# Kernel optimization log

Hardware: AMD Instinct MI355X
Metric: run time of the kernel (lower is better)

Reference implementation:

```python
import jax, jax.numpy as jnp
import numpy as np

N, D, K = 65536, 512, 4096


def setup_inputs() -> dict:
    key = jax.random.key(0)
    kx, kc = jax.random.split(key)
    x = jax.random.normal(kx, (N, D), dtype=jnp.float32)
    center = jax.random.normal(kc, (K, D), dtype=jnp.float32)
    return {"x": x, "center": center}


def squared_euclidean(x, center):
    x_sq = jnp.sum(x * x, axis=1, keepdims=True)        # [N,1]
    c_sq = jnp.sum(center * center, axis=1)             # [K]
    cross = x @ center.T                                # [N,K] GEMM
    return x_sq - 2.0 * cross + c_sq[None, :]


def reference(x, center):
    # KMeans.forward: dis_func(input, center).argmin(1)
    dist = squared_euclidean(x, center)                 # [N,K]
    return jnp.argmin(dist, axis=1)                     # [N] int32
```

## Files before the change

### kernel.cpp

```cpp
#include <hip/hip_runtime.h>

#define N_ROWS 65536
#define DIM    512
#define K_CENT 4096
#define TILE_M 256
#define TILE_N 64
#define NCT    (K_CENT / TILE_N)
#define KSTEPS 8
#define THREADS 256
#define WCAP   1024
#define WTRIG  512
#define MARGIN 22.0f
#define SCALE1 0x7F7F7F7F

typedef float  floatx4  __attribute__((ext_vector_type(4)));
typedef float  floatx16 __attribute__((ext_vector_type(16)));
typedef int    intx4    __attribute__((ext_vector_type(4)));
typedef int    intx8    __attribute__((ext_vector_type(8)));

__device__ __forceinline__ unsigned mapF(float f) {
  unsigned u = __float_as_uint(f);
  return (u & 0x80000000u) ? ~u : (u | 0x80000000u);
}
__device__ __forceinline__ float unmapF(unsigned m) {
  unsigned u = (m & 0x80000000u) ? (m ^ 0x80000000u) : ~m;
  return __uint_as_float(u);
}

__device__ __forceinline__ void gload_lds16(const void* g, void* l) {
  __builtin_amdgcn_global_load_lds(
      (const __attribute__((address_space(1))) void*)g,
      (__attribute__((address_space(3))) void*)l, 16, 0, 0);
}

__device__ __forceinline__ int pk4(float a, float b, float c, float d) {
  int r = __builtin_amdgcn_cvt_pk_fp8_f32(a, b, 0, false);
  r = __builtin_amdgcn_cvt_pk_fp8_f32(c, d, r, true);
  return r;
}

#define WAVE_LDS_FENCE() do { asm volatile("s_waitcnt lgkmcnt(0)" ::: "memory"); \
                              __builtin_amdgcn_sched_barrier(0); } while (0)

__global__ void prep_convert(const float* __restrict__ c,
                             unsigned char* __restrict__ cq, float* __restrict__ csqg) {
  size_t i = ((size_t)blockIdx.x * blockDim.x + threadIdx.x) * 16;
  if (i >= (size_t)K_CENT * DIM) return;
  floatx4 a0 = *(const floatx4*)(c + i);
  floatx4 a1 = *(const floatx4*)(c + i + 4);
  floatx4 a2 = *(const floatx4*)(c + i + 8);
  floatx4 a3 = *(const floatx4*)(c + i + 12);
  intx4 q = { pk4(a0[0],a0[1],a0[2],a0[3]), pk4(a1[0],a1[1],a1[2],a1[3]),
              pk4(a2[0],a2[1],a2[2],a2[3]), pk4(a3[0],a3[1],a3[2],a3[3]) };
  *(intx4*)(cq + i) = q;
  float s = 0.f;
#pragma unroll
  for (int e = 0; e < 4; ++e)
    s += a0[e]*a0[e] + a1[e]*a1[e] + a2[e]*a2[e] + a3[e]*a3[e];
#pragma unroll
  for (int o = 1; o < 32; o <<= 1) s += __shfl_xor(s, o, 64);
  if ((threadIdx.x & 31) == 0) csqg[i >> 9] = s;
}

__global__ __launch_bounds__(THREADS, 1)
void kmeans_argmin_pipe(const float* __restrict__ x, const float* __restrict__ cent,
                        const unsigned char* __restrict__ cq,
                        const float* __restrict__ csqg, int* __restrict__ out) {
  __shared__ __align__(16) unsigned char ringLds[4][16384];
  __shared__ __align__(16) float csqL[K_CENT];
  __shared__ unsigned sminU[TILE_M];
  __shared__ unsigned long long best[TILE_M];
  __shared__ unsigned poolK[4][WCAP];
  __shared__ float    poolS[4][WCAP];
  __shared__ int candCnt[4];

  const int t = threadIdx.x;
  const int lane = t & 63;
  const int wave = t >> 6;
  const int l31 = lane & 31;
  const int half = lane >> 5;
  const int rowBlock = blockIdx.x * TILE_M;

  sminU[t] = 0xFFFFFFFFu;
  best[t] = ~0ull;
  if (t < 4) candCnt[t] = 0;
#pragma unroll
  for (int i = 0; i < K_CENT / THREADS; ++i) csqL[t + i * THREADS] = csqg[t + i * THREADS];

  int offI0, offI1, offI2, offI3;
#pragma unroll
  for (int i = 0; i < 4; ++i) {
    int s = i * 64 + lane;
    int rS = (s >> 2) & 31;
    int row = (s >> 7) * 32 + rS;
    int cp = (s & 3) ^ ((rS >> 1) & 3);
    int v = row * DIM + cp * 16;
    if (i == 0) offI0 = v; else if (i == 1) offI1 = v;
    else if (i == 2) offI2 = v; else offI3 = v;
  }

  const int qk = half * 2;
  const int slotLo = 4 * l31 + (qk ^ ((l31 >> 1) & 3));
  const int loB = slotLo * 16;
  const int hiB = (slotLo ^ 1) * 16;
  unsigned char* ringW = ringLds[wave];

  intx8 xfA[KSTEPS], xfB[KSTEPS];
  {
    const float* xr = x + (size_t)(rowBlock + wave * 64 + l31) * DIM + half * 32;
#pragma unroll
    for (int ks = 0; ks < KSTEPS; ++ks) {
      int q[8];
#pragma unroll
      for (int j = 0; j < 8; ++j) {
        floatx4 f = *(const floatx4*)(xr + ks * 64 + j * 4);
        q[j] = pk4(f[0], f[1], f[2], f[3]);
      }
      xfA[ks] = (intx8){q[0], q[1], q[2], q[3], q[4], q[5], q[6], q[7]};
    }
    xr += (size_t)32 * DIM;
#pragma unroll
    for (int ks = 0; ks < KSTEPS; ++ks) {
      int q[8];
#pragma unroll
      for (int j = 0; j < 8; ++j) {
        floatx4 f = *(const floatx4*)(xr + ks * 64 + j * 4);
        q[j] = pk4(f[0], f[1], f[2], f[3]);
      }
      xfB[ks] = (intx8){q[0], q[1], q[2], q[3], q[4], q[5], q[6], q[7]};
    }
  }

  __syncthreads();

#pragma unroll
  for (int s = 0; s < 3; ++s) {
    unsigned char* wb = ringW + (s << 12);
    gload_lds16(cq + s * 64 + offI0, wb);
    gload_lds16(cq + s * 64 + offI1, wb + 1024);
    gload_lds16(cq + s * 64 + offI2, wb + 2048);
    gload_lds16(cq + s * 64 + offI3, wb + 3072);
  }
  unsigned sOff = 3 * 64;

  for (int ct = 0; ct < NCT; ++ct) {
    floatx16 acc00, acc01, acc10, acc11;
#pragma unroll
    for (int e = 0; e < 16; ++e) { acc00[e] = 0.f; acc01[e] = 0.f; acc10[e] = 0.f; acc11[e] = 0.f; }

#pragma unroll
    for (int p = 0; p < KSTEPS; ++p) {
      {
        unsigned char* wb = ringW + (((p + 3) & 3) << 12);
        gload_lds16(cq + sOff + offI0, wb);
        gload_lds16(cq + sOff + offI1, wb + 1024);
        gload_lds16(cq + sOff + offI2, wb + 2048);
        gload_lds16(cq + sOff + offI3, wb + 3072);
      }
      sOff += (p == 4) ? 32320u : 64u;
      asm volatile("s_waitcnt vmcnt(12)" ::: "memory");
      __builtin_amdgcn_sched_barrier(0);

      const unsigned char* rb = ringW + ((p & 3) << 12);
      intx4 lo0 = *(const intx4*)(rb + loB);
      intx4 hi0 = *(const intx4*)(rb + hiB);
      intx4 lo1 = *(const intx4*)(rb + 2048 + loB);
      intx4 hi1 = *(const intx4*)(rb + 2048 + hiB);
      asm volatile("s_waitcnt lgkmcnt(0)" ::: "memory");
      __builtin_amdgcn_sched_barrier(0);
      intx8 b0 = (intx8){lo0[0],lo0[1],lo0[2],lo0[3], hi0[0],hi0[1],hi0[2],hi0[3]};
      intx8 b1 = (intx8){lo1[0],lo1[1],lo1[2],lo1[3], hi1[0],hi1[1],hi1[2],hi1[3]};
      acc00 = __builtin_amdgcn_mfma_scale_f32_32x32x64_f8f6f4(
          b0, xfA[p], acc00, 0, 0, 0, SCALE1, 0, SCALE1);
      acc01 = __builtin_amdgcn_mfma_scale_f32_32x32x64_f8f6f4(
          b1, xfA[p], acc01, 0, 0, 0, SCALE1, 0, SCALE1);
      acc10 = __builtin_amdgcn_mfma_scale_f32_32x32x64_f8f6f4(
          b0, xfB[p], acc10, 0, 0, 0, SCALE1, 0, SCALE1);
      acc11 = __builtin_amdgcn_mfma_scale_f32_32x32x64_f8f6f4(
          b1, xfB[p], acc11, 0, 0, 0, SCALE1, 0, SCALE1);
    }

    const int ctB = ct << 6;
#pragma unroll
    for (int h = 0; h < 2; ++h) {
      const floatx16& a0 = h ? acc10 : acc00;
      const floatx16& a1 = h ? acc11 : acc01;
      const int srow = wave * 64 + h * 32 + l31;
      float mn = 3.4e38f;
#pragma unroll
      for (int gg = 0; gg < 4; ++gg) {
        floatx4 c0 = *(const floatx4*)&csqL[ctB + 8 * gg + 4 * half];
        floatx4 c1 = *(const floatx4*)&csqL[ctB + 32 + 8 * gg + 4 * half];
#pragma unroll
        for (int e = 0; e < 4; ++e) {
          mn = fminf(mn, c0[e] - 2.f * a0[4 * gg + e]);
          mn = fminf(mn, c1[e] - 2.f * a1[4 * gg + e]);
        }
      }
      mn = fminf(mn, __shfl_xor(mn, 32, 64));
      if (half == 0) atomicMin(&sminU[srow], mapF(mn));
      WAVE_LDS_FENCE();

      const float thr = unmapF(sminU[srow]) + MARGIN;
#pragma unroll
      for (int gg = 0; gg < 4; ++gg) {
        floatx4 c0 = *(const floatx4*)&csqL[ctB + 8 * gg + 4 * half];
        floatx4 c1 = *(const floatx4*)&csqL[ctB + 32 + 8 * gg + 4 * half];
#pragma unroll
        for (int e = 0; e < 4; ++e) {
          float s0 = c0[e] - 2.f * a0[4 * gg + e];
          if (s0 <= thr) {
            int k = ctB + 8 * gg + 4 * half + e;
            int idx = atomicAdd(&candCnt[wave], 1);
            if (idx < WCAP) { poolK[wave][idx] = ((unsigned)k << 8) | (unsigned)srow; poolS[wave][idx] = s0; }
          }
          float s1 = c1[e] - 2.f * a1[4 * gg + e];
          if (s1 <= thr) {
            int k = ctB + 32 + 8 * gg + 4 * half + e;
            int idx = atomicAdd(&candCnt[wave], 1);
            if (idx < WCAP) { poolK[wave][idx] = ((unsigned)k << 8) | (unsigned)srow; poolS[wave][idx] = s1; }
          }
        }
      }
    }
    WAVE_LDS_FENCE();

    if (candCnt[wave] > WTRIG) {
      int cc = candCnt[wave]; if (cc > WCAP) cc = WCAP;
      unsigned myK[16]; float myS[16]; int myN = 0;
      for (int i = lane; i < cc; i += 64) {
        int rl = poolK[wave][i] & 255;
        if (poolS[wave][i] <= unmapF(sminU[rl]) + MARGIN) {
          myK[myN] = poolK[wave][i]; myS[myN] = poolS[wave][i]; ++myN;
        }
      }
      WAVE_LDS_FENCE();
      if (lane == 0) candCnt[wave] = 0;
      WAVE_LDS_FENCE();
      int base = atomicAdd(&candCnt[wave], myN);
      for (int j = 0; j < myN; ++j) { poolK[wave][base + j] = myK[j]; poolS[wave][base + j] = myS[j]; }
      WAVE_LDS_FENCE();
    }
  }

  __syncthreads();

  const int grp = t >> 4;
  const int sl = t & 15;
  for (int w = 0; w < 4; ++w) {
    int cw = candCnt[w]; if (cw > WCAP) cw = WCAP;
    for (int ci = grp; ci < cw; ci += 16) {
      unsigned cd = poolK[w][ci];
      int rl = cd & 255;
      if (poolS[w][ci] > unmapF(sminU[rl]) + MARGIN) continue;
      int k = cd >> 8;
      const float* xr = x + (size_t)(rowBlock + rl) * DIM;
      const float* cr = cent + (size_t)k * DIM;
      double d = 0.0;
#pragma unroll
      for (int jj = 0; jj < DIM / 64; ++jj) {
        floatx4 xv = *(const floatx4*)(xr + jj * 64 + sl * 4);
        floatx4 cv = *(const floatx4*)(cr + jj * 64 + sl * 4);
#pragma unroll
        for (int e = 0; e < 4; ++e) {
          double df = (double)xv[e] - (double)cv[e];
          d += df * df;
        }
      }
#pragma unroll
      for (int off = 1; off < 16; off <<= 1) d += __shfl_xor(d, off, 64);
      if (sl == 0) {
        unsigned long long key =
            ((unsigned long long)__double_as_longlong(d) & ~0xFFFull) | (unsigned long long)k;
        atomicMin(&best[rl], key);
      }
    }
  }
  __syncthreads();
  out[rowBlock + t] = (int)(best[t] & 0xFFFull);
}

#define FB_TILE_M 128
#define FB_NKT    32
#define FB_CAP    1536
#define FB_TRIG   1024
__global__ __launch_bounds__(512, 4)
void kmeans_argmin_fb(const float* __restrict__ x, const float* __restrict__ cent,
                      int* __restrict__ out) {
  __shared__ unsigned char ldsA[FB_TILE_M * 64];
  __shared__ unsigned char ldsB[128 * 64];
  __shared__ float csq4[128][4];
  __shared__ unsigned sminU[FB_TILE_M];
  __shared__ unsigned long long best[FB_TILE_M];
  __shared__ unsigned candKey[FB_CAP];
  __shared__ float candS[FB_CAP];
  __shared__ int candCount;

  const int t = threadIdx.x;
  const int lane = t & 63;
  const int wave = t >> 6;
  const int wm = wave >> 1;
  const int wn = wave & 1;
  const int l31 = lane & 31;
  const int half = lane >> 5;
  const int rowBlock = blockIdx.x * FB_TILE_M;

  if (t < FB_TILE_M) { sminU[t] = 0xFFFFFFFFu; best[t] = ~0ull; }
  if (t == 0) candCount = 0;

  const int rS = (t >> 2) & 31;
  const int rowS = (t >> 7) * 32 + rS;
  const int offS = (((t & 3) ^ ((rS >> 1) & 3)) << 4);
  const int qk = half * 2;
  const int fragSlotBase = 4 * l31 + (qk ^ ((l31 >> 1) & 3));

  for (int kt = 0; kt < FB_NKT; ++kt) {
    const int ktBase = kt * 128;
    ((float*)csq4)[t] = 0.f;
    floatx16 acc[2];
#pragma unroll
    for (int fn = 0; fn < 2; ++fn)
#pragma unroll
      for (int e = 0; e < 16; ++e) acc[fn][e] = 0.f;

    for (int ks = 0; ks < KSTEPS; ++ks) {
      const int kd = ks * 64;
      {
        const float* gA = x + (size_t)(rowBlock + rowS) * DIM + kd + offS;
        floatx4 f0 = *(const floatx4*)gA, f1 = *(const floatx4*)(gA + 4);
        floatx4 f2 = *(const floatx4*)(gA + 8), f3 = *(const floatx4*)(gA + 12);
        intx4 q = { pk4(f0[0],f0[1],f0[2],f0[3]), pk4(f1[0],f1[1],f1[2],f1[3]),
                    pk4(f2[0],f2[1],f2[2],f2[3]), pk4(f3[0],f3[1],f3[2],f3[3]) };
        *(intx4*)(ldsA + (size_t)t * 16) = q;
      }
      {
        const float* gB = cent + (size_t)(ktBase + rowS) * DIM + kd + offS;
        floatx4 f0 = *(const floatx4*)gB, f1 = *(const floatx4*)(gB + 4);
        floatx4 f2 = *(const floatx4*)(gB + 8), f3 = *(const floatx4*)(gB + 12);
        intx4 q = { pk4(f0[0],f0[1],f0[2],f0[3]), pk4(f1[0],f1[1],f1[2],f1[3]),
                    pk4(f2[0],f2[1],f2[2],f2[3]), pk4(f3[0],f3[1],f3[2],f3[3]) };
        *(intx4*)(ldsB + (size_t)t * 16) = q;
        float s = 0.f;
#pragma unroll
        for (int e = 0; e < 4; ++e)
          s += f0[e]*f0[e] + f1[e]*f1[e] + f2[e]*f2[e] + f3[e]*f3[e];
        csq4[rowS][t & 3] += s;
      }
      __syncthreads();

      intx8 aF, bF[2];
      {
        int s0 = wm * 128 + fragSlotBase;
        intx4 lo = *(const intx4*)(ldsA + s0 * 16);
        intx4 hi = *(const intx4*)(ldsA + (s0 ^ 1) * 16);
        aF = (intx8){lo[0], lo[1], lo[2], lo[3], hi[0], hi[1], hi[2], hi[3]};
      }
#pragma unroll
      for (int fn = 0; fn < 2; ++fn) {
        int s0 = (wn * 2 + fn) * 128 + fragSlotBase;
        intx4 lo = *(const intx4*)(ldsB + s0 * 16);
        intx4 hi = *(const intx4*)(ldsB + (s0 ^ 1) * 16);
        bF[fn] = (intx8){lo[0], lo[1], lo[2], lo[3], hi[0], hi[1], hi[2], hi[3]};
      }
#pragma unroll
      for (int fn = 0; fn < 2; ++fn)
        acc[fn] = __builtin_amdgcn_mfma_scale_f32_32x32x64_f8f6f4(
            aF, bF[fn], acc[fn], 0, 0, 0, SCALE1, 0, SCALE1);
      __syncthreads();
    }

    float cs[2];
#pragma unroll
    for (int fn = 0; fn < 2; ++fn) {
      int cl = wn * 64 + fn * 32 + l31;
      cs[fn] = csq4[cl][0] + csq4[cl][1] + csq4[cl][2] + csq4[cl][3];
    }

#pragma unroll
    for (int r = 0; r < 16; ++r) {
      float v = fminf(cs[0] - 2.f * acc[0][r], cs[1] - 2.f * acc[1][r]);
      v = fminf(v, __shfl_xor(v, 1, 64));
      v = fminf(v, __shfl_xor(v, 2, 64));
      v = fminf(v, __shfl_xor(v, 4, 64));
      v = fminf(v, __shfl_xor(v, 8, 64));
      v = fminf(v, __shfl_xor(v, 16, 64));
      if (l31 == 0) {
        int srow = wm * 32 + (r & 3) + 8 * (r >> 2) + 4 * half;
        atomicMin(&sminU[srow], mapF(v));
      }
    }
    __syncthreads();

#pragma unroll
    for (int r = 0; r < 16; ++r) {
      int srow = wm * 32 + (r & 3) + 8 * (r >> 2) + 4 * half;
      float thr = unmapF(sminU[srow]) + MARGIN;
#pragma unroll
      for (int fn = 0; fn < 2; ++fn) {
        float s = cs[fn] - 2.f * acc[fn][r];
        if (s <= thr) {
          int k = ktBase + wn * 64 + fn * 32 + l31;
          int idx = atomicAdd(&candCount, 1);
          if (idx < FB_CAP) {
            candKey[idx] = ((unsigned)k << 7) | (unsigned)srow;
            candS[idx] = s;
          }
        }
      }
    }
    __syncthreads();

    if (candCount > FB_TRIG) {
      int cc = candCount; if (cc > FB_CAP) cc = FB_CAP;
      unsigned myK[4]; float myS[4]; int myN = 0;
      for (int i = t; i < cc; i += 512) {
        int rl = candKey[i] & 127;
        if (candS[i] <= unmapF(sminU[rl]) + MARGIN && myN < 4) {
          myK[myN] = candKey[i]; myS[myN] = candS[i]; ++myN;
        }
      }
      __syncthreads();
      if (t == 0) candCount = 0;
      __syncthreads();
      int base = atomicAdd(&candCount, myN);
      for (int j = 0; j < myN; ++j) { candKey[base + j] = myK[j]; candS[base + j] = myS[j]; }
      __syncthreads();
    }
  }

  int cnt = candCount; if (cnt > FB_CAP) cnt = FB_CAP;
  const int g = t >> 4;
  const int sl = t & 15;
  for (int ci = g; ci < cnt; ci += 32) {
    unsigned cd = candKey[ci];
    int rl = cd & 127;
    if (candS[ci] > unmapF(sminU[rl]) + MARGIN) continue;
    int k = cd >> 7;
    const float* xr = x + (size_t)(rowBlock + rl) * DIM;
    const float* cr = cent + (size_t)k * DIM;
    double d = 0.0;
#pragma unroll
    for (int j = 0; j < DIM / 64; ++j) {
      floatx4 xv = *(const floatx4*)(xr + j * 64 + sl * 4);
      floatx4 cv = *(const floatx4*)(cr + j * 64 + sl * 4);
#pragma unroll
      for (int e = 0; e < 4; ++e) {
        double df = (double)xv[e] - (double)cv[e];
        d += df * df;
      }
    }
#pragma unroll
    for (int off = 1; off < 16; off <<= 1) d += __shfl_xor(d, off, 64);
    if (sl == 0) {
      unsigned long long key =
          ((unsigned long long)__double_as_longlong(d) & ~0xFFFull) | (unsigned long long)k;
      atomicMin(&best[rl], key);
    }
  }
  __syncthreads();
  if (t < FB_TILE_M) out[rowBlock + t] = (int)(best[t] & 0xFFFull);
}

extern "C" void kernel_launch(void* const* d_in, const int* in_sizes, int n_in,
                              void* d_out, int out_size, void* d_ws, size_t ws_size,
                              hipStream_t stream) {
  const float* x = (const float*)d_in[0];
  const float* cent = (const float*)d_in[1];
  int* out = (int*)d_out;
  const size_t nXq = (size_t)N_ROWS * DIM;
  const size_t nCq = (size_t)K_CENT * DIM;
  const size_t nCsq = (size_t)K_CENT * sizeof(float);

  if (ws_size >= nXq + nCq + nCsq) {
    unsigned char* cq = (unsigned char*)d_ws;
    float* csqg = (float*)(cq + nCq);
    const size_t total16 = nCq / 16;
    prep_convert<<<(unsigned)((total16 + 255) / 256), 256, 0, stream>>>(cent, cq, csqg);
    kmeans_argmin_pipe<<<N_ROWS / TILE_M, THREADS, 0, stream>>>(x, cent, cq, csqg, out);
  } else {
    kmeans_argmin_fb<<<N_ROWS / FB_TILE_M, 512, 0, stream>>>(x, cent, out);
  }
}
```

Baseline: 605.8 us.

## Load fp8 centroid fragments directly into registers and halve row tile

The per-wave LDS ring filled with global_load_lds is removed. Each lane now loads its centroid fp8 fragments straight from global memory into registers, double-buffered across k-steps. The row tile drops from 256 to 128 (32 rows per wave), and launch bounds allow two blocks per CU, which cuts register and LDS use to raise occupancy. The trade-off is that every wave re-reads the centroid tiles from global/L2 with no sharing, and each x row pair now gets half the reuse of each B fragment.

```diff
diff --git a/kernel.cpp b/kernel.cpp
--- a/kernel.cpp
+++ b/kernel.cpp
@@ -3,7 +3,7 @@
 #define N_ROWS 65536
 #define DIM    512
 #define K_CENT 4096
-#define TILE_M 256
+#define TILE_M 128
 #define TILE_N 64
 #define NCT    (K_CENT / TILE_N)
 #define KSTEPS 8
@@ -25,12 +25,6 @@
 __device__ __forceinline__ float unmapF(unsigned m) {
   unsigned u = (m & 0x80000000u) ? (m ^ 0x80000000u) : ~m;
   return __uint_as_float(u);
-}
-
-__device__ __forceinline__ void gload_lds16(const void* g, void* l) {
-  __builtin_amdgcn_global_load_lds(
-      (const __attribute__((address_space(1))) void*)g,
-      (__attribute__((address_space(3))) void*)l, 16, 0, 0);
 }
 
 __device__ __forceinline__ int pk4(float a, float b, float c, float d) {
@@ -62,11 +56,40 @@
   if ((threadIdx.x & 31) == 0) csqg[i >> 9] = s;
 }
 
-__global__ __launch_bounds__(THREADS, 1)
+#define LOADP(buf, p0, p1, kb) do {                                   \
+  buf[0] = *(const intx4*)((p0) + (kb) * 64);                         \
+  buf[1] = *(const intx4*)((p0) + (kb) * 64 + 16);                    \
+  buf[2] = *(const intx4*)((p1) + (kb) * 64);                         \
+  buf[3] = *(const intx4*)((p1) + (kb) * 64 + 16);                    \
+  buf[4] = *(const intx4*)((p0) + (kb) * 64 + 64);                    \
+  buf[5] = *(const intx4*)((p0) + (kb) * 64 + 80);                    \
+  buf[6] = *(const intx4*)((p1) + (kb) * 64 + 64);                    \
+  buf[7] = *(const intx4*)((p1) + (kb) * 64 + 80);                    \
+} while (0)
+
+#define COMP(buf, kb) do {                                            \
+  intx8 b0a = (intx8){buf[0][0],buf[0][1],buf[0][2],buf[0][3],        \
+                      buf[1][0],buf[1][1],buf[1][2],buf[1][3]};       \
+  intx8 b1a = (intx8){buf[2][0],buf[2][1],buf[2][2],buf[2][3],        \
+                      buf[3][0],buf[3][1],buf[3][2],buf[3][3]};       \
+  acc0 = __builtin_amdgcn_mfma_scale_f32_32x32x64_f8f6f4(             \
+      b0a, xf[(kb)], acc0, 0, 0, 0, SCALE1, 0, SCALE1);               \
+  acc1 = __builtin_amdgcn_mfma_scale_f32_32x32x64_f8f6f4(             \
+      b1a, xf[(kb)], acc1, 0, 0, 0, SCALE1, 0, SCALE1);               \
+  intx8 b0b = (intx8){buf[4][0],buf[4][1],buf[4][2],buf[4][3],        \
+                      buf[5][0],buf[5][1],buf[5][2],buf[5][3]};       \
+  intx8 b1b = (intx8){buf[6][0],buf[6][1],buf[6][2],buf[6][3],        \
+                      buf[7][0],buf[7][1],buf[7][2],buf[7][3]};       \
+  acc0 = __builtin_amdgcn_mfma_scale_f32_32x32x64_f8f6f4(             \
+      b0b, xf[(kb) + 1], acc0, 0, 0, 0, SCALE1, 0, SCALE1);           \
+  acc1 = __builtin_amdgcn_mfma_scale_f32_32x32x64_f8f6f4(             \
+      b1b, xf[(kb) + 1], acc1, 0, 0, 0, SCALE1, 0, SCALE1);           \
+} while (0)
+
+__global__ __launch_bounds__(THREADS, 2)
 void kmeans_argmin_pipe(const float* __restrict__ x, const float* __restrict__ cent,
                         const unsigned char* __restrict__ cq,
                         const float* __restrict__ csqg, int* __restrict__ out) {
-  __shared__ __align__(16) unsigned char ringLds[4][16384];
   __shared__ __align__(16) float csqL[K_CENT];
   __shared__ unsigned sminU[TILE_M];
   __shared__ unsigned long long best[TILE_M];
@@ -80,34 +103,16 @@
   const int l31 = lane & 31;
   const int half = lane >> 5;
   const int rowBlock = blockIdx.x * TILE_M;
-
-  sminU[t] = 0xFFFFFFFFu;
-  best[t] = ~0ull;
+  const int srow = wave * 32 + l31;
+
+  if (t < TILE_M) { sminU[t] = 0xFFFFFFFFu; best[t] = ~0ull; }
   if (t < 4) candCnt[t] = 0;
 #pragma unroll
   for (int i = 0; i < K_CENT / THREADS; ++i) csqL[t + i * THREADS] = csqg[t + i * THREADS];
 
-  int offI0, offI1, offI2, offI3;
-#pragma unroll
-  for (int i = 0; i < 4; ++i) {
-    int s = i * 64 + lane;
-    int rS = (s >> 2) & 31;
-    int row = (s >> 7) * 32 + rS;
-    int cp = (s & 3) ^ ((rS >> 1) & 3);
-    int v = row * DIM + cp * 16;
-    if (i == 0) offI0 = v; else if (i == 1) offI1 = v;
-    else if (i == 2) offI2 = v; else offI3 = v;
-  }
-
-  const int qk = half * 2;
-  const int slotLo = 4 * l31 + (qk ^ ((l31 >> 1) & 3));
-  const int loB = slotLo * 16;
-  const int hiB = (slotLo ^ 1) * 16;
-  unsigned char* ringW = ringLds[wave];
-
-  intx8 xfA[KSTEPS], xfB[KSTEPS];
+  intx8 xf[KSTEPS];
   {
-    const float* xr = x + (size_t)(rowBlock + wave * 64 + l31) * DIM + half * 32;
+    const float* xr = x + (size_t)(rowBlock + srow) * DIM + half * 32;
 #pragma unroll
     for (int ks = 0; ks < KSTEPS; ++ks) {
       int q[8];
@@ -116,110 +121,63 @@
         floatx4 f = *(const floatx4*)(xr + ks * 64 + j * 4);
         q[j] = pk4(f[0], f[1], f[2], f[3]);
       }
-      xfA[ks] = (intx8){q[0], q[1], q[2], q[3], q[4], q[5], q[6], q[7]};
-    }
-    xr += (size_t)32 * DIM;
-#pragma unroll
-    for (int ks = 0; ks < KSTEPS; ++ks) {
-      int q[8];
-#pragma unroll
-      for (int j = 0; j < 8; ++j) {
-        floatx4 f = *(const floatx4*)(xr + ks * 64 + j * 4);
-        q[j] = pk4(f[0], f[1], f[2], f[3]);
-      }
-      xfB[ks] = (intx8){q[0], q[1], q[2], q[3], q[4], q[5], q[6], q[7]};
-    }
-  }
-
+      xf[ks] = (intx8){q[0], q[1], q[2], q[3], q[4], q[5], q[6], q[7]};
+    }
+  }
   __syncthreads();
 
-#pragma unroll
-  for (int s = 0; s < 3; ++s) {
-    unsigned char* wb = ringW + (s << 12);
-    gload_lds16(cq + s * 64 + offI0, wb);
-    gload_lds16(cq + s * 64 + offI1, wb + 1024);
-    gload_lds16(cq + s * 64 + offI2, wb + 2048);
-    gload_lds16(cq + s * 64 + offI3, wb + 3072);
-  }
-  unsigned sOff = 3 * 64;
+  const unsigned char* b0p = cq + (size_t)l31 * DIM + half * 32;
+  const unsigned char* b1p = b0p + (size_t)32 * DIM;
+
+  intx4 bufA[8], bufB[8];
+  LOADP(bufA, b0p, b1p, 0);
 
   for (int ct = 0; ct < NCT; ++ct) {
-    floatx16 acc00, acc01, acc10, acc11;
-#pragma unroll
-    for (int e = 0; e < 16; ++e) { acc00[e] = 0.f; acc01[e] = 0.f; acc10[e] = 0.f; acc11[e] = 0.f; }
-
-#pragma unroll
-    for (int p = 0; p < KSTEPS; ++p) {
-      {
-        unsigned char* wb = ringW + (((p + 3) & 3) << 12);
-        gload_lds16(cq + sOff + offI0, wb);
-        gload_lds16(cq + sOff + offI1, wb + 1024);
-        gload_lds16(cq + sOff + offI2, wb + 2048);
-        gload_lds16(cq + sOff + offI3, wb + 3072);
-      }
-      sOff += (p == 4) ? 32320u : 64u;
-      asm volatile("s_waitcnt vmcnt(12)" ::: "memory");
-      __builtin_amdgcn_sched_barrier(0);
-
-      const unsigned char* rb = ringW + ((p & 3) << 12);
-      intx4 lo0 = *(const intx4*)(rb + loB);
-      intx4 hi0 = *(const intx4*)(rb + hiB);
-      intx4 lo1 = *(const intx4*)(rb + 2048 + loB);
-      intx4 hi1 = *(const intx4*)(rb + 2048 + hiB);
-      asm volatile("s_waitcnt lgkmcnt(0)" ::: "memory");
-      __builtin_amdgcn_sched_barrier(0);
-      intx8 b0 = (intx8){lo0[0],lo0[1],lo0[2],lo0[3], hi0[0],hi0[1],hi0[2],hi0[3]};
-      intx8 b1 = (intx8){lo1[0],lo1[1],lo1[2],lo1[3], hi1[0],hi1[1],hi1[2],hi1[3]};
-      acc00 = __builtin_amdgcn_mfma_scale_f32_32x32x64_f8f6f4(
-          b0, xfA[p], acc00, 0, 0, 0, SCALE1, 0, SCALE1);
-      acc01 = __builtin_amdgcn_mfma_scale_f32_32x32x64_f8f6f4(
-          b1, xfA[p], acc01, 0, 0, 0, SCALE1, 0, SCALE1);
-      acc10 = __builtin_amdgcn_mfma_scale_f32_32x32x64_f8f6f4(
-          b0, xfB[p], acc10, 0, 0, 0, SCALE1, 0, SCALE1);
-      acc11 = __builtin_amdgcn_mfma_scale_f32_32x32x64_f8f6f4(
-          b1, xfB[p], acc11, 0, 0, 0, SCALE1, 0, SCALE1);
-    }
+    floatx16 acc0, acc1;
+#pragma unroll
+    for (int e = 0; e < 16; ++e) { acc0[e] = 0.f; acc1[e] = 0.f; }
+
+    LOADP(bufB, b0p, b1p, 2);  COMP(bufA, 0);
+    LOADP(bufA, b0p, b1p, 4);  COMP(bufB, 2);
+    LOADP(bufB, b0p, b1p, 6);  COMP(bufA, 4);
+    b0p += (size_t)TILE_N * DIM;
+    b1p += (size_t)TILE_N * DIM;
+    LOADP(bufA, b0p, b1p, 0);  COMP(bufB, 6);
 
     const int ctB = ct << 6;
-#pragma unroll
-    for (int h = 0; h < 2; ++h) {
-      const floatx16& a0 = h ? acc10 : acc00;
-      const floatx16& a1 = h ? acc11 : acc01;
-      const int srow = wave * 64 + h * 32 + l31;
-      float mn = 3.4e38f;
-#pragma unroll
-      for (int gg = 0; gg < 4; ++gg) {
-        floatx4 c0 = *(const floatx4*)&csqL[ctB + 8 * gg + 4 * half];
-        floatx4 c1 = *(const floatx4*)&csqL[ctB + 32 + 8 * gg + 4 * half];
-#pragma unroll
-        for (int e = 0; e < 4; ++e) {
-          mn = fminf(mn, c0[e] - 2.f * a0[4 * gg + e]);
-          mn = fminf(mn, c1[e] - 2.f * a1[4 * gg + e]);
-        }
-      }
-      mn = fminf(mn, __shfl_xor(mn, 32, 64));
-      if (half == 0) atomicMin(&sminU[srow], mapF(mn));
-      WAVE_LDS_FENCE();
-
-      const float thr = unmapF(sminU[srow]) + MARGIN;
-#pragma unroll
-      for (int gg = 0; gg < 4; ++gg) {
-        floatx4 c0 = *(const floatx4*)&csqL[ctB + 8 * gg + 4 * half];
-        floatx4 c1 = *(const floatx4*)&csqL[ctB + 32 + 8 * gg + 4 * half];
-#pragma unroll
-        for (int e = 0; e < 4; ++e) {
-          float s0 = c0[e] - 2.f * a0[4 * gg + e];
-          if (s0 <= thr) {
-            int k = ctB + 8 * gg + 4 * half + e;
-            int idx = atomicAdd(&candCnt[wave], 1);
-            if (idx < WCAP) { poolK[wave][idx] = ((unsigned)k << 8) | (unsigned)srow; poolS[wave][idx] = s0; }
-          }
-          float s1 = c1[e] - 2.f * a1[4 * gg + e];
-          if (s1 <= thr) {
-            int k = ctB + 32 + 8 * gg + 4 * half + e;
-            int idx = atomicAdd(&candCnt[wave], 1);
-            if (idx < WCAP) { poolK[wave][idx] = ((unsigned)k << 8) | (unsigned)srow; poolS[wave][idx] = s1; }
-          }
+    float mn = 3.4e38f;
+#pragma unroll
+    for (int gg = 0; gg < 4; ++gg) {
+      floatx4 c0 = *(const floatx4*)&csqL[ctB + 8 * gg + 4 * half];
+      floatx4 c1 = *(const floatx4*)&csqL[ctB + 32 + 8 * gg + 4 * half];
+#pragma unroll
+      for (int e = 0; e < 4; ++e) {
+        mn = fminf(mn, c0[e] - 2.f * acc0[4 * gg + e]);
+        mn = fminf(mn, c1[e] - 2.f * acc1[4 * gg + e]);
+      }
+    }
+    mn = fminf(mn, __shfl_xor(mn, 32, 64));
+    if (half == 0) atomicMin(&sminU[srow], mapF(mn));
+    WAVE_LDS_FENCE();
+
+    const float thr = unmapF(sminU[srow]) + MARGIN;
+#pragma unroll
+    for (int gg = 0; gg < 4; ++gg) {
+      floatx4 c0 = *(const floatx4*)&csqL[ctB + 8 * gg + 4 * half];
+      floatx4 c1 = *(const floatx4*)&csqL[ctB + 32 + 8 * gg + 4 * half];
+#pragma unroll
+      for (int e = 0; e < 4; ++e) {
+        float s0 = c0[e] - 2.f * acc0[4 * gg + e];
+        if (s0 <= thr) {
+          int k = ctB + 8 * gg + 4 * half + e;
+          int idx = atomicAdd(&candCnt[wave], 1);
+          if (idx < WCAP) { poolK[wave][idx] = ((unsigned)k << 8) | (unsigned)srow; poolS[wave][idx] = s0; }
+        }
+        float s1 = c1[e] - 2.f * acc1[4 * gg + e];
+        if (s1 <= thr) {
+          int k = ctB + 32 + 8 * gg + 4 * half + e;
+          int idx = atomicAdd(&candCnt[wave], 1);
+          if (idx < WCAP) { poolK[wave][idx] = ((unsigned)k << 8) | (unsigned)srow; poolS[wave][idx] = s1; }
         }
       }
     }
@@ -277,7 +235,7 @@
     }
   }
   __syncthreads();
-  out[rowBlock + t] = (int)(best[t] & 0xFFFull);
+  if (t < TILE_M) out[rowBlock + t] = (int)(best[t] & 0xFFFull);
 }
 
 #define FB_TILE_M 128
```

Measured after the change: 725.0 us. 19.7% more time.
